# Kernel tuning notes

Measured on AMD Instinct MI355X. Metric: run time of the kernel, lower is better.

Reference implementation:

```python
import jax, jax.numpy as jnp
import numpy as np

NUM_HEADS = 16


def setup_inputs() -> dict:
    key = jax.random.key(0)
    ks = jax.random.split(key, 9)
    B, Nq, Nk = 2, 2048, 2048
    qd, kd, vd = 1024, 1024, 1024
    s = 0.02
    return {
        "query": jax.random.normal(ks[0], (B, Nq, qd), jnp.float32),
        "key": jax.random.normal(ks[1], (B, Nk, kd), jnp.float32),
        "value": jax.random.normal(ks[2], (B, Nk, vd), jnp.float32),
        "Wq": jax.random.normal(ks[3], (qd, qd), jnp.float32) * s,
        "bq": jnp.zeros((qd,), jnp.float32),
        "Wk": jax.random.normal(ks[4], (kd, qd), jnp.float32) * s,
        "bk": jnp.zeros((qd,), jnp.float32),
        "Wv": jax.random.normal(ks[5], (vd, vd), jnp.float32) * s,
        "bv": jnp.zeros((vd,), jnp.float32),
    }


def _split_heads(x, num_heads):
    B, N, D = x.shape
    return x.reshape(B, N, num_heads, D // num_heads).transpose(0, 2, 1, 3)  # [B,H,N,depth]


def reference(query, key, value, Wq, bq, Wk, bk, Wv, bv):
    H = NUM_HEADS
    q = _split_heads(query @ Wq + bq, H)   # [B,H,Nq,dq]
    k = _split_heads(key @ Wk + bk, H)     # [B,H,Nk,dq]
    v = _split_heads(value @ Wv + bv, H)   # [B,H,Nk,dv]
    q_depth = q.shape[-1]
    scores = jnp.einsum('bhqd,bhkd->bhqk', q, k) / jnp.sqrt(jnp.float32(q_depth))
    scores = scores - jnp.max(scores, axis=-1, keepdims=True)
    attn = jax.nn.softmax(scores, axis=-1)  # [B,H,Nq,Nk]
    context = jnp.einsum('bhqk,bhkd->bhqd', attn, v)
    B, _, Nq, dv = context.shape
    context = context.transpose(0, 2, 1, 3).reshape(B, Nq, H * dv)
    return (context, attn)
```

## Files before the change

kernel.cpp:

```cpp
#include <hip/hip_runtime.h>
#include <hip/hip_bf16.h>
#include <stdint.h>

typedef __attribute__((ext_vector_type(4))) float floatx4;
typedef __attribute__((ext_vector_type(8))) short shortx8;

#define NTOK 2048
#define DMODEL 1024
#define NHEAD 16
#define DHEAD 64
#define BATCH 2

static __device__ __forceinline__ unsigned short f2bf(float f) {
    union { float f; unsigned int u; } v; v.f = f;
    return (unsigned short)((v.u + 0x7FFFu + ((v.u >> 16) & 1u)) >> 16);
}

static __device__ __forceinline__ floatx4 mfma16(shortx8 a, shortx8 b, floatx4 c) {
    return __builtin_amdgcn_mfma_f32_16x16x32_bf16(a, b, c, 0, 0, 0);
}

static __device__ __forceinline__ void gl_lds16(const unsigned short* g, unsigned short* l) {
    __builtin_amdgcn_global_load_lds(
        (const __attribute__((address_space(1))) unsigned int*)g,
        (__attribute__((address_space(3))) unsigned int*)l, 16, 0, 0);
}

#define C1 0.18033688f

__global__ void cast_x_kernel(const float* __restrict__ q, const float* __restrict__ k,
                              const float* __restrict__ v,
                              unsigned short* __restrict__ oq, unsigned short* __restrict__ ok,
                              unsigned short* __restrict__ ov) {
    const float* src = blockIdx.y == 0 ? q : (blockIdx.y == 1 ? k : v);
    unsigned short* dst = blockIdx.y == 0 ? oq : (blockIdx.y == 1 ? ok : ov);
    int i = (blockIdx.x * 256 + threadIdx.x) * 8;
    floatx4 a = *(const floatx4*)(src + i);
    floatx4 b = *(const floatx4*)(src + i + 4);
    union { shortx8 s; unsigned short u[8]; } o;
    o.u[0] = f2bf(a[0]); o.u[1] = f2bf(a[1]); o.u[2] = f2bf(a[2]); o.u[3] = f2bf(a[3]);
    o.u[4] = f2bf(b[0]); o.u[5] = f2bf(b[1]); o.u[6] = f2bf(b[2]); o.u[7] = f2bf(b[3]);
    *(shortx8*)(dst + i) = o.s;
}

__global__ void transpose_w_kernel(const float* __restrict__ wq, const float* __restrict__ wk,
                                   const float* __restrict__ wv,
                                   unsigned short* __restrict__ tq, unsigned short* __restrict__ tk,
                                   unsigned short* __restrict__ tv) {
    __shared__ float tile[32][33];
    const float* W = blockIdx.z == 0 ? wq : (blockIdx.z == 1 ? wk : wv);
    unsigned short* T = blockIdx.z == 0 ? tq : (blockIdx.z == 1 ? tk : tv);
    int tx = threadIdx.x, ty = threadIdx.y;
    int bx = blockIdx.x, by = blockIdx.y;
#pragma unroll
    for (int j = 0; j < 4; j++)
        tile[ty + j * 8][tx] = W[(by * 32 + ty + j * 8) * DMODEL + bx * 32 + tx];
    __syncthreads();
#pragma unroll
    for (int j = 0; j < 4; j++)
        T[(bx * 32 + ty + j * 8) * DMODEL + by * 32 + tx] = f2bf(tile[tx][ty + j * 8]);
}

__launch_bounds__(256)
__global__ void proj_gemm_kernel(const unsigned short* __restrict__ xq, const unsigned short* __restrict__ xk,
                                 const unsigned short* __restrict__ xv,
                                 const unsigned short* __restrict__ tq, const unsigned short* __restrict__ tk,
                                 const unsigned short* __restrict__ tv,
                                 const float* __restrict__ bq, const float* __restrict__ bk,
                                 const float* __restrict__ bv,
                                 unsigned short* __restrict__ qh, unsigned short* __restrict__ kh,
                                 unsigned short* __restrict__ vt) {
    int z = blockIdx.z;
    const unsigned short* X = z == 0 ? xq : (z == 1 ? xk : xv);
    const unsigned short* W = z == 0 ? tq : (z == 1 ? tk : tv);
    const float* bias = z == 0 ? bq : (z == 1 ? bk : bv);

    __shared__ unsigned short As[128 * 32];
    __shared__ unsigned short Bs[128 * 32];

    int t = threadIdx.x;
    int lane = t & 63, w = t >> 6;
    int wr = w >> 1, wc = w & 1;
    int r = lane & 15, g = lane >> 4;
    int m0 = blockIdx.y * 128, n0 = blockIdx.x * 128;

    floatx4 acc[4][4];
#pragma unroll
    for (int i = 0; i < 4; i++)
#pragma unroll
        for (int j = 0; j < 4; j++) acc[i][j] = (floatx4){0.f, 0.f, 0.f, 0.f};

    for (int kt = 0; kt < DMODEL; kt += 32) {
#pragma unroll
        for (int i = 0; i < 2; i++) {
            int idx = t + 256 * i;
            int row = idx >> 2, c8 = (idx & 3) * 8;
            gl_lds16(X + (size_t)(m0 + row) * DMODEL + kt + c8, As + idx * 8);
            gl_lds16(W + (size_t)(n0 + row) * DMODEL + kt + c8, Bs + idx * 8);
        }
        __syncthreads();
        shortx8 a[4], b[4];
#pragma unroll
        for (int f = 0; f < 4; f++) {
            a[f] = *(const shortx8*)(As + (wr * 64 + f * 16 + r) * 32 + g * 8);
            b[f] = *(const shortx8*)(Bs + (wc * 64 + f * 16 + r) * 32 + g * 8);
        }
#pragma unroll
        for (int fm = 0; fm < 4; fm++)
#pragma unroll
            for (int fn = 0; fn < 4; fn++)
                acc[fm][fn] = mfma16(a[fm], b[fn], acc[fm][fn]);
        __syncthreads();
    }

    unsigned short* dstQK = (z == 0) ? qh : kh;
#pragma unroll
    for (int fm = 0; fm < 4; fm++) {
#pragma unroll
        for (int fn = 0; fn < 4; fn++) {
            int n = n0 + wc * 64 + fn * 16 + r;
            float bval = bias[n];
            int h = n >> 6, d = n & 63;
#pragma unroll
            for (int reg = 0; reg < 4; reg++) {
                int m = m0 + wr * 64 + fm * 16 + g * 4 + reg;
                int bb = m >> 11, tok = m & 2047;
                unsigned short o = f2bf(acc[fm][fn][reg] + bval);
                if (z < 2)
                    dstQK[(((size_t)(bb * NHEAD + h) * NTOK + tok) * DHEAD) + d] = o;
                else
                    vt[(((size_t)(bb * NHEAD + h) * DHEAD + d) * NTOK) + tok] = o;
            }
        }
    }
}

__launch_bounds__(256, 4)
__global__ void attn2_kernel(const unsigned short* __restrict__ Qh,
                             const unsigned short* __restrict__ Kh,
                             const unsigned short* __restrict__ Vt,
                             float* __restrict__ ctx, float* __restrict__ attn) {
    __shared__ __align__(16) unsigned short Kst[2][4096];
    __shared__ __align__(16) unsigned short Aux[2][4096];

    int t = threadIdx.x, lane = t & 63, w = t >> 6, r = lane & 15, g = lane >> 4;

    int bid = blockIdx.x;
    int xcd = bid & 7;
    int j = bid >> 3;
    int bh = xcd * 4 + (j & 3);
    int qb = j >> 2;

    int q0 = qb * 64 + w * 16;
    int qrow = q0 + r;
    int rs = r & 7;

    const unsigned short* Qp = Qh + ((size_t)bh * NTOK + q0) * DHEAD;
    const unsigned short* Kbase = Kh + (size_t)bh * NTOK * DHEAD;
    const unsigned short* Vbase = Vt + (size_t)bh * DHEAD * NTOK;

    shortx8 qf0 = *(const shortx8*)(Qp + r * DHEAD + g * 8);
    shortx8 qf1 = *(const shortx8*)(Qp + r * DHEAD + 32 + g * 8);

    const floatx4 zero = (floatx4){0.f, 0.f, 0.f, 0.f};

    auto STK = [&](int b, int it) {
#pragma unroll
        for (int p = 0; p < 2; ++p) {
            int row = p * 32 + (t >> 3);
            int cb = (t & 7) ^ ((t >> 3) & 7);
            gl_lds16(Kbase + ((size_t)(it * 64 + row)) * DHEAD + cb * 8,
                     Kst[b] + p * 2048 + t * 8);
        }
    };
    auto STV = [&](int b, int it) {
#pragma unroll
        for (int p = 0; p < 2; ++p) {
            int row = p * 32 + (t >> 3);
            int cb = (t & 7) ^ ((t >> 3) & 7);
            gl_lds16(Vbase + (size_t)row * NTOK + it * 64 + cb * 8,
                     Aux[b] + p * 2048 + t * 8);
        }
    };
    auto KF = [&](int b, int tq, int h) -> shortx8 {
        return *(const shortx8*)(Kst[b] + (tq * 16 + r) * 64 + 8 * (((h * 4) + g) ^ rs));
    };
    auto VF = [&](int b, int dt, int h4) -> shortx8 {
        return *(const shortx8*)(Aux[b] + (dt * 16 + r) * 64 + 8 * ((h4 + g) ^ rs));
    };

    float tot;
    {
        floatx4 pv0 = zero, pv1 = zero, pv2 = zero, pv3 = zero;
        float sm = 0.f;
        const bool hi = (g >= 2);
        const int srcA = (r + ((g & 1) << 5)) << 2;
        const int srcB = srcA + 64;

        STK(0, 0); STV(0, 0);
        __syncthreads();
        for (int it = 0; it < 32; ++it) {
            int cur = it & 1, nxt = cur ^ 1;
            if (it < 31) { STK(nxt, it + 1); STV(nxt, it + 1); }
#pragma unroll
            for (int half = 0; half < 2; ++half) {
                unsigned int p01t0, p23t0, p01t1, p23t1;
                {
                    floatx4 sc = mfma16(KF(cur, half * 2, 0), qf0, zero);
                    sc = mfma16(KF(cur, half * 2, 1), qf1, sc);
                    float e0 = exp2f(C1 * sc[0]), e1 = exp2f(C1 * sc[1]);
                    float e2 = exp2f(C1 * sc[2]), e3 = exp2f(C1 * sc[3]);
                    sm += (e0 + e1) + (e2 + e3);
                    asm("v_cvt_pk_bf16_f32 %0, %1, %2" : "=v"(p01t0) : "v"(e0), "v"(e1));
                    asm("v_cvt_pk_bf16_f32 %0, %1, %2" : "=v"(p23t0) : "v"(e2), "v"(e3));
                }
                {
                    floatx4 sc = mfma16(KF(cur, half * 2 + 1, 0), qf0, zero);
                    sc = mfma16(KF(cur, half * 2 + 1, 1), qf1, sc);
                    float e0 = exp2f(C1 * sc[0]), e1 = exp2f(C1 * sc[1]);
                    float e2 = exp2f(C1 * sc[2]), e3 = exp2f(C1 * sc[3]);
                    sm += (e0 + e1) + (e2 + e3);
                    asm("v_cvt_pk_bf16_f32 %0, %1, %2" : "=v"(p01t1) : "v"(e0), "v"(e1));
                    asm("v_cvt_pk_bf16_f32 %0, %1, %2" : "=v"(p23t1) : "v"(e2), "v"(e3));
                }
                int b0a = __builtin_amdgcn_ds_bpermute(srcA, (int)p01t0);
                int b0b = __builtin_amdgcn_ds_bpermute(srcA, (int)p01t1);
                int b1a = __builtin_amdgcn_ds_bpermute(srcA, (int)p23t0);
                int b1b = __builtin_amdgcn_ds_bpermute(srcA, (int)p23t1);
                int b2a = __builtin_amdgcn_ds_bpermute(srcB, (int)p01t0);
                int b2b = __builtin_amdgcn_ds_bpermute(srcB, (int)p01t1);
                int b3a = __builtin_amdgcn_ds_bpermute(srcB, (int)p23t0);
                int b3b = __builtin_amdgcn_ds_bpermute(srcB, (int)p23t1);
                union { unsigned int u[4]; shortx8 s8; } pbu;
                pbu.u[0] = (unsigned)(hi ? b0b : b0a);
                pbu.u[1] = (unsigned)(hi ? b1b : b1a);
                pbu.u[2] = (unsigned)(hi ? b2b : b2a);
                pbu.u[3] = (unsigned)(hi ? b3b : b3a);
                pv0 = mfma16(VF(cur, 0, half * 4), pbu.s8, pv0);
                pv1 = mfma16(VF(cur, 1, half * 4), pbu.s8, pv1);
                pv2 = mfma16(VF(cur, 2, half * 4), pbu.s8, pv2);
                pv3 = mfma16(VF(cur, 3, half * 4), pbu.s8, pv3);
            }
            __syncthreads();
        }
        tot = sm;
        tot += __shfl_xor(tot, 16, 64);
        tot += __shfl_xor(tot, 32, 64);
        float inv = 1.0f / tot;
        float* ctx_row =
            ctx + ((size_t)((bh >> 4) * NTOK + qrow)) * DMODEL + (bh & 15) * DHEAD + g * 4;
        *(floatx4*)(ctx_row) = pv0 * inv;
        *(floatx4*)(ctx_row + 16) = pv1 * inv;
        *(floatx4*)(ctx_row + 32) = pv2 * inv;
        *(floatx4*)(ctx_row + 48) = pv3 * inv;
    }

    float nl2s = -__log2f(tot);

    {
        float(*pw)[64] = (float(*)[64])((char*)Aux + (size_t)w * 4096);
        float* attn_base = attn + ((size_t)bh * NTOK + q0) * NTOK;

        STK(0, 0);
        __syncthreads();
        for (int it = 0; it < 32; ++it) {
            int cur = it & 1, nxt = cur ^ 1;
            if (it < 31) STK(nxt, it + 1);
            int kk0 = it * 64;
#pragma unroll
            for (int tq = 0; tq < 4; ++tq) {
                floatx4 sc = mfma16(KF(cur, tq, 0), qf0, zero);
                sc = mfma16(KF(cur, tq, 1), qf1, sc);
                float e0 = exp2f(fmaf(C1, sc[0], nl2s));
                float e1 = exp2f(fmaf(C1, sc[1], nl2s));
                float e2 = exp2f(fmaf(C1, sc[2], nl2s));
                float e3 = exp2f(fmaf(C1, sc[3], nl2s));
                int x_ = (tq * 4 + g) ^ r;
                *(floatx4*)&pw[r][4 * x_] = (floatx4){e0, e1, e2, e3};
            }
#pragma unroll
            for (int sID = 0; sID < 4; ++sID) {
                int row = 4 * sID + g;
                floatx4 vvv = *(const floatx4*)&pw[row][4 * (r ^ row)];
                __builtin_nontemporal_store(
                    vvv, (floatx4*)(attn_base + (size_t)row * NTOK + kk0 + 4 * r));
            }
            __syncthreads();
        }
    }
}

extern "C" void kernel_launch(void* const* d_in, const int* in_sizes, int n_in,
                              void* d_out, int out_size, void* d_ws, size_t ws_size,
                              hipStream_t stream) {
    const float* query = (const float*)d_in[0];
    const float* key   = (const float*)d_in[1];
    const float* value = (const float*)d_in[2];
    const float* Wq = (const float*)d_in[3];
    const float* bq = (const float*)d_in[4];
    const float* Wk = (const float*)d_in[5];
    const float* bk = (const float*)d_in[6];
    const float* Wv = (const float*)d_in[7];
    const float* bv = (const float*)d_in[8];

    const size_t NX = (size_t)BATCH * NTOK * DMODEL;
    const size_t NW = (size_t)DMODEL * DMODEL;

    unsigned short* ws = (unsigned short*)d_ws;
    unsigned short* Xq = ws;
    unsigned short* Xk = Xq + NX;
    unsigned short* Xv = Xk + NX;
    unsigned short* Tq = Xv + NX;
    unsigned short* Tk = Tq + NW;
    unsigned short* Tv = Tk + NW;
    unsigned short* Qh = Tv + NW;
    unsigned short* Kh = Qh + NX;
    unsigned short* Vt = Kh + NX;

    float* ctx = (float*)d_out;
    float* attn = ctx + NX;

    cast_x_kernel<<<dim3(2048, 3), 256, 0, stream>>>(query, key, value, Xq, Xk, Xv);
    transpose_w_kernel<<<dim3(32, 32, 3), dim3(32, 8), 0, stream>>>(Wq, Wk, Wv, Tq, Tk, Tv);
    proj_gemm_kernel<<<dim3(8, 32, 3), 256, 0, stream>>>(Xq, Xk, Xv, Tq, Tk, Tv,
                                                         bq, bk, bv, Qh, Kh, Vt);
    attn2_kernel<<<dim3(1024), 256, 0, stream>>>(Qh, Kh, Vt, ctx, attn);
}
```

Baseline: 277.1 us.

## Pair query blocks per workgroup to overlap attn writes with next block's context pass

Each workgroup now handles two 64-row query blocks. The second block's context/softmax-sum pass shares K-tile loads with, and is interleaved with, the first block's normalized attention-probability write pass. This halves the number of K sweeps per query block (three sweeps for two blocks instead of four) and overlaps the store-heavy attn write with MFMA/exp work. The cost is half as many workgroups (512), more registers for the second Q fragment set, and a dedicated 16KB LDS buffer for the transpose staging, which can reduce occupancy.

```diff
diff --git a/kernel.cpp b/kernel.cpp
--- a/kernel.cpp
+++ b/kernel.cpp
@@ -136,12 +136,13 @@
 }
 
 __launch_bounds__(256, 4)
-__global__ void attn2_kernel(const unsigned short* __restrict__ Qh,
-                             const unsigned short* __restrict__ Kh,
-                             const unsigned short* __restrict__ Vt,
-                             float* __restrict__ ctx, float* __restrict__ attn) {
+__global__ void attn_pair_kernel(const unsigned short* __restrict__ Qh,
+                                 const unsigned short* __restrict__ Kh,
+                                 const unsigned short* __restrict__ Vt,
+                                 float* __restrict__ ctx, float* __restrict__ attn) {
     __shared__ __align__(16) unsigned short Kst[2][4096];
-    __shared__ __align__(16) unsigned short Aux[2][4096];
+    __shared__ __align__(16) unsigned short Vst[2][4096];
+    __shared__ __align__(16) float Pfl[4][16][64];
 
     int t = threadIdx.x, lane = t & 63, w = t >> 6, r = lane & 15, g = lane >> 4;
 
@@ -149,20 +150,26 @@
     int xcd = bid & 7;
     int j = bid >> 3;
     int bh = xcd * 4 + (j & 3);
-    int qb = j >> 2;
-
-    int q0 = qb * 64 + w * 16;
-    int qrow = q0 + r;
+    int pr = j >> 2;
+    int q00 = (pr * 2) * 64 + w * 16;
+    int q01 = q00 + 64;
     int rs = r & 7;
 
-    const unsigned short* Qp = Qh + ((size_t)bh * NTOK + q0) * DHEAD;
     const unsigned short* Kbase = Kh + (size_t)bh * NTOK * DHEAD;
     const unsigned short* Vbase = Vt + (size_t)bh * DHEAD * NTOK;
-
-    shortx8 qf0 = *(const shortx8*)(Qp + r * DHEAD + g * 8);
-    shortx8 qf1 = *(const shortx8*)(Qp + r * DHEAD + 32 + g * 8);
+    const unsigned short* Qp0 = Qh + ((size_t)bh * NTOK + q00) * DHEAD;
+    const unsigned short* Qp1 = Qh + ((size_t)bh * NTOK + q01) * DHEAD;
+
+    shortx8 qf0_0 = *(const shortx8*)(Qp0 + r * DHEAD + g * 8);
+    shortx8 qf1_0 = *(const shortx8*)(Qp0 + r * DHEAD + 32 + g * 8);
+    shortx8 qf0_1 = *(const shortx8*)(Qp1 + r * DHEAD + g * 8);
+    shortx8 qf1_1 = *(const shortx8*)(Qp1 + r * DHEAD + 32 + g * 8);
 
     const floatx4 zero = (floatx4){0.f, 0.f, 0.f, 0.f};
+    const bool hi = (g >= 2);
+    const int srcA = (r + ((g & 1) << 5)) << 2;
+    const int srcB = srcA + 64;
+    float(*pw)[64] = Pfl[w];
 
     auto STK = [&](int b, int it) {
 #pragma unroll
@@ -179,115 +186,147 @@
             int row = p * 32 + (t >> 3);
             int cb = (t & 7) ^ ((t >> 3) & 7);
             gl_lds16(Vbase + (size_t)row * NTOK + it * 64 + cb * 8,
-                     Aux[b] + p * 2048 + t * 8);
+                     Vst[b] + p * 2048 + t * 8);
         }
     };
     auto KF = [&](int b, int tq, int h) -> shortx8 {
         return *(const shortx8*)(Kst[b] + (tq * 16 + r) * 64 + 8 * (((h * 4) + g) ^ rs));
     };
     auto VF = [&](int b, int dt, int h4) -> shortx8 {
-        return *(const shortx8*)(Aux[b] + (dt * 16 + r) * 64 + 8 * ((h4 + g) ^ rs));
+        return *(const shortx8*)(Vst[b] + (dt * 16 + r) * 64 + 8 * ((h4 + g) ^ rs));
     };
 
-    float tot;
+#define CTX_ITER(cur, QA, QB, SM, PV0, PV1, PV2, PV3)                          \
+    {                                                                          \
+        _Pragma("unroll")                                                      \
+        for (int half = 0; half < 2; ++half) {                                 \
+            unsigned int p01t0, p23t0, p01t1, p23t1;                           \
+            {                                                                  \
+                floatx4 sc = mfma16(KF(cur, half * 2, 0), QA, zero);           \
+                sc = mfma16(KF(cur, half * 2, 1), QB, sc);                     \
+                float e0 = exp2f(C1 * sc[0]), e1 = exp2f(C1 * sc[1]);          \
+                float e2 = exp2f(C1 * sc[2]), e3 = exp2f(C1 * sc[3]);          \
+                SM += (e0 + e1) + (e2 + e3);                                   \
+                asm("v_cvt_pk_bf16_f32 %0, %1, %2" : "=v"(p01t0) : "v"(e0), "v"(e1)); \
+                asm("v_cvt_pk_bf16_f32 %0, %1, %2" : "=v"(p23t0) : "v"(e2), "v"(e3)); \
+            }                                                                  \
+            {                                                                  \
+                floatx4 sc = mfma16(KF(cur, half * 2 + 1, 0), QA, zero);       \
+                sc = mfma16(KF(cur, half * 2 + 1, 1), QB, sc);                 \
+                float e0 = exp2f(C1 * sc[0]), e1 = exp2f(C1 * sc[1]);          \
+                float e2 = exp2f(C1 * sc[2]), e3 = exp2f(C1 * sc[3]);          \
+                SM += (e0 + e1) + (e2 + e3);                                   \
+                asm("v_cvt_pk_bf16_f32 %0, %1, %2" : "=v"(p01t1) : "v"(e0), "v"(e1)); \
+                asm("v_cvt_pk_bf16_f32 %0, %1, %2" : "=v"(p23t1) : "v"(e2), "v"(e3)); \
+            }                                                                  \
+            int b0a = __builtin_amdgcn_ds_bpermute(srcA, (int)p01t0);          \
+            int b0b = __builtin_amdgcn_ds_bpermute(srcA, (int)p01t1);          \
+            int b1a = __builtin_amdgcn_ds_bpermute(srcA, (int)p23t0);          \
+            int b1b = __builtin_amdgcn_ds_bpermute(srcA, (int)p23t1);          \
+            int b2a = __builtin_amdgcn_ds_bpermute(srcB, (int)p01t0);          \
+            int b2b = __builtin_amdgcn_ds_bpermute(srcB, (int)p01t1);          \
+            int b3a = __builtin_amdgcn_ds_bpermute(srcB, (int)p23t0);          \
+            int b3b = __builtin_amdgcn_ds_bpermute(srcB, (int)p23t1);          \
+            union { unsigned int u[4]; shortx8 s8; } pbu;                      \
+            pbu.u[0] = (unsigned)(hi ? b0b : b0a);                             \
+            pbu.u[1] = (unsigned)(hi ? b1b : b1a);                             \
+            pbu.u[2] = (unsigned)(hi ? b2b : b2a);                             \
+            pbu.u[3] = (unsigned)(hi ? b3b : b3a);                             \
+            PV0 = mfma16(VF(cur, 0, half * 4), pbu.s8, PV0);                   \
+            PV1 = mfma16(VF(cur, 1, half * 4), pbu.s8, PV1);                   \
+            PV2 = mfma16(VF(cur, 2, half * 4), pbu.s8, PV2);                   \
+            PV3 = mfma16(VF(cur, 3, half * 4), pbu.s8, PV3);                   \
+        }                                                                      \
+    }
+
+#define WRT_ITER(cur, QA, QB, NL2S, ABASE, KK0)                                \
+    {                                                                          \
+        _Pragma("unroll")                                                      \
+        for (int tq = 0; tq < 4; ++tq) {                                       \
+            floatx4 sc = mfma16(KF(cur, tq, 0), QA, zero);                     \
+            sc = mfma16(KF(cur, tq, 1), QB, sc);                               \
+            float e0 = exp2f(fmaf(C1, sc[0], NL2S));                           \
+            float e1 = exp2f(fmaf(C1, sc[1], NL2S));                           \
+            float e2 = exp2f(fmaf(C1, sc[2], NL2S));                           \
+            float e3 = exp2f(fmaf(C1, sc[3], NL2S));                           \
+            int x_ = (tq * 4 + g) ^ r;                                         \
+            *(floatx4*)&pw[r][4 * x_] = (floatx4){e0, e1, e2, e3};             \
+        }                                                                      \
+        _Pragma("unroll")                                                      \
+        for (int sID = 0; sID < 4; ++sID) {                                    \
+            int row = 4 * sID + g;                                             \
+            floatx4 vvv = *(const floatx4*)&pw[row][4 * (r ^ row)];            \
+            __builtin_nontemporal_store(                                       \
+                vvv, (floatx4*)((ABASE) + (size_t)row * NTOK + (KK0) + 4 * r)); \
+        }                                                                      \
+    }
+
+    float* attn_base0 = attn + ((size_t)bh * NTOK + q00) * NTOK;
+    float* attn_base1 = attn + ((size_t)bh * NTOK + q01) * NTOK;
+
+    float nl2s0;
     {
         floatx4 pv0 = zero, pv1 = zero, pv2 = zero, pv3 = zero;
-        float sm = 0.f;
-        const bool hi = (g >= 2);
-        const int srcA = (r + ((g & 1) << 5)) << 2;
-        const int srcB = srcA + 64;
-
+        float sm0 = 0.f;
         STK(0, 0); STV(0, 0);
         __syncthreads();
         for (int it = 0; it < 32; ++it) {
             int cur = it & 1, nxt = cur ^ 1;
             if (it < 31) { STK(nxt, it + 1); STV(nxt, it + 1); }
-#pragma unroll
-            for (int half = 0; half < 2; ++half) {
-                unsigned int p01t0, p23t0, p01t1, p23t1;
-                {
-                    floatx4 sc = mfma16(KF(cur, half * 2, 0), qf0, zero);
-                    sc = mfma16(KF(cur, half * 2, 1), qf1, sc);
-                    float e0 = exp2f(C1 * sc[0]), e1 = exp2f(C1 * sc[1]);
-                    float e2 = exp2f(C1 * sc[2]), e3 = exp2f(C1 * sc[3]);
-                    sm += (e0 + e1) + (e2 + e3);
-                    asm("v_cvt_pk_bf16_f32 %0, %1, %2" : "=v"(p01t0) : "v"(e0), "v"(e1));
-                    asm("v_cvt_pk_bf16_f32 %0, %1, %2" : "=v"(p23t0) : "v"(e2), "v"(e3));
-                }
-                {
-                    floatx4 sc = mfma16(KF(cur, half * 2 + 1, 0), qf0, zero);
-                    sc = mfma16(KF(cur, half * 2 + 1, 1), qf1, sc);
-                    float e0 = exp2f(C1 * sc[0]), e1 = exp2f(C1 * sc[1]);
-                    float e2 = exp2f(C1 * sc[2]), e3 = exp2f(C1 * sc[3]);
-                    sm += (e0 + e1) + (e2 + e3);
-                    asm("v_cvt_pk_bf16_f32 %0, %1, %2" : "=v"(p01t1) : "v"(e0), "v"(e1));
-                    asm("v_cvt_pk_bf16_f32 %0, %1, %2" : "=v"(p23t1) : "v"(e2), "v"(e3));
-                }
-                int b0a = __builtin_amdgcn_ds_bpermute(srcA, (int)p01t0);
-                int b0b = __builtin_amdgcn_ds_bpermute(srcA, (int)p01t1);
-                int b1a = __builtin_amdgcn_ds_bpermute(srcA, (int)p23t0);
-                int b1b = __builtin_amdgcn_ds_bpermute(srcA, (int)p23t1);
-                int b2a = __builtin_amdgcn_ds_bpermute(srcB, (int)p01t0);
-                int b2b = __builtin_amdgcn_ds_bpermute(srcB, (int)p01t1);
-                int b3a = __builtin_amdgcn_ds_bpermute(srcB, (int)p23t0);
-                int b3b = __builtin_amdgcn_ds_bpermute(srcB, (int)p23t1);
-                union { unsigned int u[4]; shortx8 s8; } pbu;
-                pbu.u[0] = (unsigned)(hi ? b0b : b0a);
-                pbu.u[1] = (unsigned)(hi ? b1b : b1a);
-                pbu.u[2] = (unsigned)(hi ? b2b : b2a);
-                pbu.u[3] = (unsigned)(hi ? b3b : b3a);
-                pv0 = mfma16(VF(cur, 0, half * 4), pbu.s8, pv0);
-                pv1 = mfma16(VF(cur, 1, half * 4), pbu.s8, pv1);
-                pv2 = mfma16(VF(cur, 2, half * 4), pbu.s8, pv2);
-                pv3 = mfma16(VF(cur, 3, half * 4), pbu.s8, pv3);
-            }
+            CTX_ITER(cur, qf0_0, qf1_0, sm0, pv0, pv1, pv2, pv3);
             __syncthreads();
         }
-        tot = sm;
+        float tot = sm0;
         tot += __shfl_xor(tot, 16, 64);
         tot += __shfl_xor(tot, 32, 64);
         float inv = 1.0f / tot;
-        float* ctx_row =
-            ctx + ((size_t)((bh >> 4) * NTOK + qrow)) * DMODEL + (bh & 15) * DHEAD + g * 4;
+        nl2s0 = -__log2f(tot);
+        float* ctx_row = ctx + ((size_t)((bh >> 4) * NTOK + q00 + r)) * DMODEL +
+                         (bh & 15) * DHEAD + g * 4;
         *(floatx4*)(ctx_row) = pv0 * inv;
         *(floatx4*)(ctx_row + 16) = pv1 * inv;
         *(floatx4*)(ctx_row + 32) = pv2 * inv;
         *(floatx4*)(ctx_row + 48) = pv3 * inv;
     }
 
-    float nl2s = -__log2f(tot);
-
+    float nl2s1;
     {
-        float(*pw)[64] = (float(*)[64])((char*)Aux + (size_t)w * 4096);
-        float* attn_base = attn + ((size_t)bh * NTOK + q0) * NTOK;
-
+        floatx4 pv0 = zero, pv1 = zero, pv2 = zero, pv3 = zero;
+        float sm1 = 0.f;
+        STK(0, 0); STV(0, 0);
+        __syncthreads();
+        for (int it = 0; it < 32; ++it) {
+            int cur = it & 1, nxt = cur ^ 1;
+            if (it < 31) { STK(nxt, it + 1); STV(nxt, it + 1); }
+            CTX_ITER(cur, qf0_1, qf1_1, sm1, pv0, pv1, pv2, pv3);
+            WRT_ITER(cur, qf0_0, qf1_0, nl2s0, attn_base0, it * 64);
+            __syncthreads();
+        }
+        float tot = sm1;
+        tot += __shfl_xor(tot, 16, 64);
+        tot += __shfl_xor(tot, 32, 64);
+        float inv = 1.0f / tot;
+        nl2s1 = -__log2f(tot);
+        float* ctx_row = ctx + ((size_t)((bh >> 4) * NTOK + q01 + r)) * DMODEL +
+                         (bh & 15) * DHEAD + g * 4;
+        *(floatx4*)(ctx_row) = pv0 * inv;
+        *(floatx4*)(ctx_row + 16) = pv1 * inv;
+        *(floatx4*)(ctx_row + 32) = pv2 * inv;
+        *(floatx4*)(ctx_row + 48) = pv3 * inv;
+    }
+
+    {
         STK(0, 0);
         __syncthreads();
         for (int it = 0; it < 32; ++it) {
             int cur = it & 1, nxt = cur ^ 1;
             if (it < 31) STK(nxt, it + 1);
-            int kk0 = it * 64;
-#pragma unroll
-            for (int tq = 0; tq < 4; ++tq) {
-                floatx4 sc = mfma16(KF(cur, tq, 0), qf0, zero);
-                sc = mfma16(KF(cur, tq, 1), qf1, sc);
-                float e0 = exp2f(fmaf(C1, sc[0], nl2s));
-                float e1 = exp2f(fmaf(C1, sc[1], nl2s));
-                float e2 = exp2f(fmaf(C1, sc[2], nl2s));
-                float e3 = exp2f(fmaf(C1, sc[3], nl2s));
-                int x_ = (tq * 4 + g) ^ r;
-                *(floatx4*)&pw[r][4 * x_] = (floatx4){e0, e1, e2, e3};
-            }
-#pragma unroll
-            for (int sID = 0; sID < 4; ++sID) {
-                int row = 4 * sID + g;
-                floatx4 vvv = *(const floatx4*)&pw[row][4 * (r ^ row)];
-                __builtin_nontemporal_store(
-                    vvv, (floatx4*)(attn_base + (size_t)row * NTOK + kk0 + 4 * r));
-            }
+            WRT_ITER(cur, qf0_1, qf1_1, nl2s1, attn_base1, it * 64);
             __syncthreads();
         }
     }
+#undef CTX_ITER
+#undef WRT_ITER
 }
 
 extern "C" void kernel_launch(void* const* d_in, const int* in_sizes, int n_in,
@@ -324,5 +363,5 @@
     transpose_w_kernel<<<dim3(32, 32, 3), dim3(32, 8), 0, stream>>>(Wq, Wk, Wv, Tq, Tk, Tv);
     proj_gemm_kernel<<<dim3(8, 32, 3), 256, 0, stream>>>(Xq, Xk, Xv, Tq, Tk, Tv,
                                                          bq, bk, bv, Qh, Kh, Vt);
-    attn2_kernel<<<dim3(1024), 256, 0, stream>>>(Qh, Kh, Vt, ctx, attn);
-}
+    attn_pair_kernel<<<dim3(512), 256, 0, stream>>>(Qh, Kh, Vt, ctx, attn);
+}
```

Measured after the change: 258.6 us. 6.7% less time.
